# Kernel optimization log

Measured on AMD Instinct MI355X. Metric: run time of the kernel, lower is better.

## Reference

```python
import jax, jax.numpy as jnp
from jax import lax
import numpy as np

V = 4096                 # variants per batch
NUM_READ_FEATURES = 24
NUM_INFO_FEATURES = 10
REF_LEN = 25             # ref sequence length (one-hot over ACGT)
CONV_C = 32
KERN = 3
READ_E = 128
INFO_E = 64
SEQ_E = 64
EMB = READ_E + INFO_E + SEQ_E   # 256, matches hstack of read/info/seq embeddings
FFN = 512                # self_attention_hidden_dimension
NUM_BLOCKS = 2           # num_self_attention_layers
AGG_H = 256
AGG_OUT = 128
WEIGHT_RANGE = 0.2


def _init_params(key):
    ks = iter(jax.random.split(key, 40))
    def lin(din, dout):
        w = jax.random.normal(next(ks), (din, dout), jnp.float32) / np.float32(np.sqrt(din))
        return w, jnp.zeros((dout,), jnp.float32)
    p = {}
    p['read_w1'], p['read_b1'] = lin(NUM_READ_FEATURES, READ_E)
    p['read_w2'], p['read_b2'] = lin(READ_E, READ_E)
    p['info_w1'], p['info_b1'] = lin(NUM_INFO_FEATURES, INFO_E)
    p['info_w2'], p['info_b2'] = lin(INFO_E, INFO_E)
    p['conv_w'] = jax.random.normal(next(ks), (CONV_C, 4, KERN), jnp.float32) / np.float32(np.sqrt(4 * KERN))
    p['conv_b'] = jnp.zeros((CONV_C,), jnp.float32)
    flat = CONV_C * (REF_LEN - KERN + 1)
    p['seq_w'], p['seq_b'] = lin(flat, SEQ_E)
    p['blk_w1'] = jax.random.normal(next(ks), (NUM_BLOCKS, EMB, FFN), jnp.float32) / np.float32(np.sqrt(EMB))
    p['blk_b1'] = jnp.zeros((NUM_BLOCKS, FFN), jnp.float32)
    p['blk_wg'] = jax.random.normal(next(ks), (NUM_BLOCKS, EMB, FFN), jnp.float32) / np.float32(np.sqrt(EMB))
    p['blk_bg'] = jnp.zeros((NUM_BLOCKS, FFN), jnp.float32)
    p['blk_w2'] = jax.random.normal(next(ks), (NUM_BLOCKS, FFN, EMB), jnp.float32) / np.float32(np.sqrt(FFN))
    p['blk_b2'] = jnp.zeros((NUM_BLOCKS, EMB), jnp.float32)
    p['agg_w1'], p['agg_b1'] = lin(EMB, AGG_H)
    p['agg_w2'], p['agg_b2'] = lin(AGG_H, AGG_OUT)
    return p


def setup_inputs() -> dict:
    rng = np.random.default_rng(0)
    ref_counts_np = rng.integers(5, 45, size=V)
    alt_counts_np = rng.integers(2, 23, size=V)
    total_ref = int(ref_counts_np.sum())
    total_alt = int(alt_counts_np.sum())
    key = jax.random.key(0)
    k1, k2, k3, kp = jax.random.split(key, 4)
    reads_2d = jax.random.normal(k1, (total_ref + total_alt, NUM_READ_FEATURES), jnp.float32)
    info_2d = jax.random.normal(k2, (V, NUM_INFO_FEATURES), jnp.float32)
    base_idx = rng.integers(0, 4, size=(V, REF_LEN))
    ref_seq_oh = jnp.asarray(np.eye(4, dtype=np.float32)[base_idx].transpose(0, 2, 1))  # [V,4,L]
    alt_u = jax.random.uniform(k3, (total_alt,), jnp.float32)  # replaces torch.rand for alt weights
    inp = {
        'reads_2d': reads_2d, 'info_2d': info_2d, 'ref_seq_oh': ref_seq_oh, 'alt_u': alt_u,
        'ref_counts': jnp.asarray(ref_counts_np, jnp.int32),
        'alt_counts': jnp.asarray(alt_counts_np, jnp.int32),
    }
    inp.update(_init_params(kp))
    return inp


def _mlp2(x, w1, b1, w2, b2):
    return jax.nn.relu(x @ w1 + b1) @ w2 + b2


def _forward(reads_2d, info_2d, ref_seq_oh, alt_u,
             read_w1, read_b1, read_w2, read_b2,
             info_w1, info_b1, info_w2, info_b2,
             conv_w, conv_b, seq_w, seq_b,
             blk_w1, blk_b1, blk_wg, blk_bg, blk_w2, blk_b2,
             agg_w1, agg_b1, agg_w2, agg_b2,
             ref_counts, alt_counts):
    total_alt = alt_u.shape[0]
    total_ref = reads_2d.shape[0] - total_alt
    # per-read and per-variant embeddings
    read_re = _mlp2(reads_2d, read_w1, read_b1, read_w2, read_b2)          # [R, READ_E]
    info_ve = _mlp2(info_2d, info_w1, info_b1, info_w2, info_b2)           # [V, INFO_E]
    conv = lax.conv_general_dilated(ref_seq_oh, conv_w, window_strides=(1,), padding='VALID',
                                    dimension_numbers=('NCH', 'OIH', 'NCH'))
    conv = jax.nn.relu(conv + conv_b[None, :, None])                       # [V, C, L-K+1]
    seq_ve = conv.reshape(conv.shape[0], -1) @ seq_w + seq_b               # [V, SEQ_E]
    info_seq_ve = jnp.concatenate([info_ve, seq_ve], axis=1)               # [V, INFO_E+SEQ_E]
    # ragged broadcast: variant-level rows repeated per read (repeat_interleave)
    ref_ids = jnp.repeat(jnp.arange(V), ref_counts, total_repeat_length=total_ref)
    alt_ids = jnp.repeat(jnp.arange(V), alt_counts, total_repeat_length=total_alt)
    ref_x = jnp.concatenate([read_re[:total_ref], info_seq_ve[ref_ids]], axis=1)   # [total_ref, EMB]
    alt_x = jnp.concatenate([read_re[total_ref:], info_seq_ve[alt_ids]], axis=1)   # [total_alt, EMB]
    ref_cf = ref_counts.astype(ref_x.dtype)[:, None]
    alt_cf = alt_counts.astype(alt_x.dtype)[:, None]
    # gated ref/alt encoder: per-read MLP cross-gated by the other set's segment mean
    for i in range(NUM_BLOCKS):
        ref_mean = jax.ops.segment_sum(ref_x, ref_ids, num_segments=V) / ref_cf
        alt_mean = jax.ops.segment_sum(alt_x, alt_ids, num_segments=V) / alt_cf
        def blk(x, gate_src):
            h = jax.nn.relu(x @ blk_w1[i] + blk_b1[i]) * jax.nn.sigmoid(gate_src @ blk_wg[i] + blk_bg[i])
            return h @ blk_w2[i] + blk_b2[i]
        ref_x = ref_x + blk(ref_x, alt_mean[ref_ids])
        alt_x = alt_x + blk(alt_x, ref_mean[alt_ids])
    # normalized weighted segment sums over alt reads (utils.sums_over_rows)
    w_r = 1.0 + WEIGHT_RANGE * (1.0 - 2.0 * alt_u)                          # [total_alt]
    wt_sums_v = jax.ops.segment_sum(w_r, alt_ids, num_segments=V)           # [V]
    norm_w = w_r / wt_sums_v[alt_ids]
    alt_means_ve = jax.ops.segment_sum(alt_x * norm_w[:, None], alt_ids, num_segments=V)  # [V, EMB]
    return _mlp2(alt_means_ve, agg_w1, agg_b1, agg_w2, agg_b2)              # [V, AGG_OUT]


def reference(reads_2d, info_2d, ref_seq_oh, alt_u,
              read_w1, read_b1, read_w2, read_b2,
              info_w1, info_b1, info_w2, info_b2,
              conv_w, conv_b, seq_w, seq_b,
              blk_w1, blk_b1, blk_wg, blk_bg, blk_w2, blk_b2,
              agg_w1, agg_b1, agg_w2, agg_b2,
              ref_counts, alt_counts):
    return _forward(reads_2d, info_2d, ref_seq_oh, alt_u,
                    read_w1, read_b1, read_w2, read_b2,
                    info_w1, info_b1, info_w2, info_b2,
                    conv_w, conv_b, seq_w, seq_b,
                    blk_w1, blk_b1, blk_wg, blk_bg, blk_w2, blk_b2,
                    agg_w1, agg_b1, agg_w2, agg_b2,
                    ref_counts, alt_counts)
```

## Files before the change

kernel.cpp:

```cpp
#include <hip/hip_runtime.h>
#include <math.h>


typedef short short8 __attribute__((ext_vector_type(8)));
typedef __bf16 bf16x8 __attribute__((ext_vector_type(8)));
typedef float f32x4 __attribute__((ext_vector_type(4)));

__device__ inline unsigned short f2bf(float f) {
    unsigned u = __builtin_bit_cast(unsigned, f);
    u += 0x7fffu + ((u >> 16) & 1u);
    return (unsigned short)(u >> 16);
}
__device__ inline float bf2f(unsigned short u) {
    unsigned v = ((unsigned)u) << 16;
    return __builtin_bit_cast(float, v);
}

__device__ inline f32x4 mfma16(short8 a, short8 b, f32x4 c) {
    return __builtin_amdgcn_mfma_f32_16x16x32_bf16(
        __builtin_bit_cast(bf16x8, a), __builtin_bit_cast(bf16x8, b), c, 0, 0, 0);
}

__device__ inline int lds_idx(int row, int k, int Kp, int mask) {
    return row * Kp + (k ^ ((row & mask) << 3));
}

__global__ __launch_bounds__(256) void scan_counts(const int* __restrict__ cnt,
                                                   int* __restrict__ off, int V) {
    __shared__ int part[256];
    int t = threadIdx.x;
    int items = (V + 255) >> 8;
    int base = t * items;
    int s = 0;
    for (int i = 0; i < items; i++) {
        int idx = base + i;
        if (idx < V) s += cnt[idx];
    }
    part[t] = s;
    __syncthreads();
    for (int d = 1; d < 256; d <<= 1) {
        int v = (t >= d) ? part[t - d] : 0;
        __syncthreads();
        part[t] += v;
        __syncthreads();
    }
    int run = (t == 0) ? 0 : part[t - 1];
    for (int i = 0; i < items; i++) {
        int idx = base + i;
        if (idx < V) {
            off[idx] = run;
            run += cnt[idx];
        }
    }
    if (t == 255) off[V] = part[255];
}

__global__ void fill_ids(const int* __restrict__ off_r, int* __restrict__ rid_r,
                         const int* __restrict__ off_a, int* __restrict__ rid_a, int V) {
    int v = blockIdx.x * blockDim.x + threadIdx.x;
    if (v < V) {
        int s = off_r[v], e = off_r[v + 1];
        for (int r = s; r < e; r++) rid_r[r] = v;
    } else if (v < 2 * V) {
        int u = v - V;
        int s = off_a[u], e = off_a[u + 1];
        for (int r = s; r < e; r++) rid_a[r] = u;
    }
}

__global__ void pack_w(const float* __restrict__ src, unsigned short* __restrict__ dst,
                       int Ksrc, int K, int N, int ctN) {
    int idx = blockIdx.x * 256 + threadIdx.x;
    if (idx >= N * K) return;
    int e = idx & 7;
    int lane = (idx >> 3) & 63;
    int li = lane & 15, lg = lane >> 4;
    int r = idx >> 9;
    int ct = r % ctN;
    int r2 = r / ctN;
    int sN = K >> 5;
    int s = r2 % sN;
    int strip = r2 / sN;
    int n = strip * (ctN << 4) + (ct << 4) + li;
    int k = (s << 5) + (lg << 3) + e;
    dst[idx] = (k < Ksrc) ? f2bf(src[(size_t)k * N + n]) : (unsigned short)0;
}

__global__ void reads_to_bf(const float* __restrict__ reads, unsigned short* __restrict__ out,
                            int R) {
    int idx = blockIdx.x * 256 + threadIdx.x;
    if (idx >= R * 32) return;
    int r = idx >> 5, k = idx & 31;
    out[idx] = (k < 24) ? f2bf(reads[(size_t)r * 24 + k]) : (unsigned short)0;
}

template <int EPI>
__global__ __launch_bounds__(256, 4) void gemm_bf16(
        const unsigned short* __restrict__ A, const unsigned short* __restrict__ Bp,
        const float* __restrict__ bias, void* __restrict__ C0, void* __restrict__ C1,
        int M, int K, int mask, int ldc, int TR) {
    extern __shared__ unsigned short As[];
    const int m0 = blockIdx.x * 64, n0 = blockIdx.y * 64;
    const int tid = threadIdx.x;
    const int kc = K >> 3;
    for (int i = tid; i < (kc << 6); i += 256) {
        int r = i / kc, k8 = (i - r * kc) << 3;
        short8 v = {0, 0, 0, 0, 0, 0, 0, 0};
        if (m0 + r < M) v = *(const short8*)(A + (size_t)(m0 + r) * K + k8);
        *(short8*)&As[lds_idx(r, k8, K, mask)] = v;
    }
    __syncthreads();
    const int wid = tid >> 6, lane = tid & 63;
    const int lr = lane & 15, lg = lane >> 4;
    f32x4 acc[4];
#pragma unroll
    for (int ct = 0; ct < 4; ++ct) acc[ct] = f32x4{0.f, 0.f, 0.f, 0.f};
    const unsigned short* Bb = Bp + (size_t)blockIdx.y * ((size_t)K << 6) + (lane << 3);
    const int nk = K >> 5;
    for (int s = 0; s < nk; ++s) {
        int k0 = (s << 5) + (lg << 3);
        short8 af = *(const short8*)&As[lds_idx((wid << 4) + lr, k0, K, mask)];
#pragma unroll
        for (int ct = 0; ct < 4; ++ct) {
            short8 bf = *(const short8*)(Bb + (s << 11) + (ct << 9));
            acc[ct] = mfma16(af, bf, acc[ct]);
        }
    }
#pragma unroll
    for (int ct = 0; ct < 4; ++ct) {
        int c = n0 + (ct << 4) + lr;
        float bb = bias[c];
#pragma unroll
        for (int q = 0; q < 4; ++q) {
            int rg = m0 + (wid << 4) + (lg << 2) + q;
            if (rg >= M) continue;
            float v = acc[ct][q] + bb;
            if (EPI == 0) {
                ((float*)C0)[(size_t)rg * ldc + c] = v;
            } else if (EPI == 1) {
                ((unsigned short*)C0)[(size_t)rg * ldc + c] = f2bf(fmaxf(v, 0.f));
            } else if (EPI == 2) {
                ((unsigned short*)C0)[(size_t)rg * ldc + c] = f2bf(1.f / (1.f + __expf(-v)));
            } else {
                unsigned short* base = (rg < TR) ? ((unsigned short*)C0 + (size_t)rg * ldc)
                                                 : ((unsigned short*)C1 + (size_t)(rg - TR) * ldc);
                base[c] = f2bf(v);
            }
        }
    }
}

__global__ __launch_bounds__(128) void variant_embed(
        const float* __restrict__ info2d, const float* __restrict__ oh,
        const float* __restrict__ iw1, const float* __restrict__ ib1,
        const float* __restrict__ iw2, const float* __restrict__ ib2,
        const float* __restrict__ cw, const float* __restrict__ cb,
        const float* __restrict__ sw, const float* __restrict__ sb,
        unsigned short* __restrict__ isv, int V) {
    __shared__ float iw1s[10 * 64], iw2s[64 * 64], ib1s[64], ib2s[64];
    __shared__ float cws[32 * 4 * 3], cbs[32];
    __shared__ float ohs[100], cv[736], his[64], infs[10];
    int v = blockIdx.x;
    int t = threadIdx.x;
    for (int i = t; i < 640; i += 128) iw1s[i] = iw1[i];
    for (int i = t; i < 4096; i += 128) iw2s[i] = iw2[i];
    for (int i = t; i < 384; i += 128) cws[i] = cw[i];
    if (t < 64) { ib1s[t] = ib1[t]; ib2s[t] = ib2[t]; }
    if (t < 32) cbs[t] = cb[t];
    for (int i = t; i < 100; i += 128) ohs[i] = oh[(size_t)v * 100 + i];
    if (t < 10) infs[t] = info2d[(size_t)v * 10 + t];
    __syncthreads();
    for (int j = t; j < 736; j += 128) {
        int c = j / 23, p = j - c * 23;
        float a = cbs[c];
#pragma unroll
        for (int i = 0; i < 4; i++)
#pragma unroll
            for (int k = 0; k < 3; k++)
                a += cws[(c * 4 + i) * 3 + k] * ohs[i * 25 + p + k];
        cv[j] = fmaxf(a, 0.f);
    }
    if (t < 64) {
        float h = ib1s[t];
#pragma unroll
        for (int k = 0; k < 10; k++) h += infs[k] * iw1s[k * 64 + t];
        his[t] = fmaxf(h, 0.f);
    }
    __syncthreads();
    if (t < 64) {
        float o = ib2s[t];
        for (int k = 0; k < 64; k++) o += his[k] * iw2s[k * 64 + t];
        isv[(size_t)v * 128 + t] = f2bf(o);
    } else {
        int tt = t - 64;
        float s = sb[tt];
        for (int j = 0; j < 736; j++) s += cv[j] * sw[j * 64 + tt];
        isv[(size_t)v * 128 + 64 + tt] = f2bf(s);
    }
}

__global__ void gather_isv_bf(const uint4* __restrict__ isv4,
                              const int* __restrict__ rid_r, const int* __restrict__ rid_a,
                              uint4* __restrict__ xref4, uint4* __restrict__ xalt4,
                              int TR, int TA) {
    long idx = (long)blockIdx.x * blockDim.x + threadIdx.x;
    long total = (long)(TR + TA) * 16;
    if (idx >= total) return;
    int r = (int)(idx >> 4);
    int j = (int)(idx & 15);
    if (r < TR)
        xref4[(size_t)r * 32 + 16 + j] = isv4[(size_t)rid_r[r] * 16 + j];
    else {
        int r2 = r - TR;
        xalt4[(size_t)r2 * 32 + 16 + j] = isv4[(size_t)rid_a[r2] * 16 + j];
    }
}

__global__ __launch_bounds__(256) void seg_mean_bf(
        const unsigned short* __restrict__ xref, const int* __restrict__ off_r,
        const unsigned short* __restrict__ xalt, const int* __restrict__ off_a,
        unsigned short* __restrict__ m2, int V) {
    __shared__ float red[2048];
    int b = blockIdx.x;
    int t = threadIdx.x;
    const unsigned short* x;
    const int* off;
    unsigned short* out;
    int v;
    if (b < V) { x = xref; off = off_r; out = m2 + (size_t)(V + b) * 256; v = b; }
    else { x = xalt; off = off_a; out = m2 + (size_t)(b - V) * 256; v = b - V; }
    int s = off[v], e = off[v + 1];
    int g = t >> 5, c8 = (t & 31) << 3;
    float a[8] = {0.f, 0.f, 0.f, 0.f, 0.f, 0.f, 0.f, 0.f};
    for (int r = s + g; r < e; r += 8) {
        short8 vv = *(const short8*)(x + (size_t)r * 256 + c8);
#pragma unroll
        for (int k = 0; k < 8; k++) a[k] += bf2f((unsigned short)vv[k]);
    }
#pragma unroll
    for (int k = 0; k < 8; k++) red[g * 256 + c8 + k] = a[k];
    __syncthreads();
    float acc = red[t];
#pragma unroll
    for (int g2 = 1; g2 < 8; g2++) acc += red[g2 * 256 + t];
    out[t] = f2bf(acc / (float)(e - s));
}

__global__ __launch_bounds__(512, 4) void fused_block(
        unsigned short* __restrict__ xref, unsigned short* __restrict__ xalt,
        const unsigned short* __restrict__ W1p,
        const unsigned short* __restrict__ W2p,
        const float* __restrict__ b1, const float* __restrict__ b2,
        const unsigned short* __restrict__ gate_r, const unsigned short* __restrict__ gate_a,
        const int* __restrict__ rid_r, const int* __restrict__ rid_a,
        int TR, int TA, int ntr) {
    __shared__ unsigned short U[64 * 512];
    __shared__ int rid_s[64];
    float* OutF = (float*)U;
    const int nwg = gridDim.x;
    const int bid0 = blockIdx.x;
    const int q8 = nwg >> 3, r8 = nwg & 7;
    const int xcd = bid0 & 7;
    const int bid = (xcd < r8 ? xcd * (q8 + 1) : r8 * (q8 + 1) + (xcd - r8) * q8)
                    + (bid0 >> 3);
    const bool isref = bid < ntr;
    const int m0 = (isref ? bid : bid - ntr) * 64;
    const int M = isref ? TR : TA;
    unsigned short* x = isref ? xref : xalt;
    const unsigned short* gate = isref ? gate_r : gate_a;
    const int* rid = isref ? rid_r : rid_a;
    const int tid = threadIdx.x;
    if (tid < 64) rid_s[tid] = (m0 + tid < M) ? rid[m0 + tid] : 0;
#pragma unroll
    for (int u = 0; u < 4; ++u) {
        int i = tid + (u << 9);
        int r = i >> 5, j = i & 31;
        short8 v = {0, 0, 0, 0, 0, 0, 0, 0};
        if (m0 + r < M)
            v = *(const short8*)(x + (size_t)(m0 + r) * 256 + ((j ^ (r & 15)) << 3));
        *(short8*)&U[r * 256 + (j << 3)] = v;
    }
    __syncthreads();
    const int wid = tid >> 6, lane = tid & 63;
    const int li = lane & 15, lg = lane >> 4;
    const int ns = wid << 6;
    f32x4 acc1[4][4];
#pragma unroll
    for (int i = 0; i < 4; ++i)
#pragma unroll
        for (int j = 0; j < 4; ++j) acc1[i][j] = f32x4{0.f, 0.f, 0.f, 0.f};
    const unsigned short* W1b = W1p + ((size_t)wid << 14) + (lane << 3);
    short8 awc[4], awn[4];
#pragma unroll
    for (int ct = 0; ct < 4; ++ct) awc[ct] = *(const short8*)(W1b + (ct << 9));
#pragma unroll
    for (int s = 0; s < 8; ++s) {
        if (s < 7) {
#pragma unroll
            for (int ct = 0; ct < 4; ++ct)
                awn[ct] = *(const short8*)(W1b + ((s + 1) << 11) + (ct << 9));
        }
        int k0 = (s << 5) + (lg << 3);
        __builtin_amdgcn_s_setprio(1);
#pragma unroll
        for (int rt = 0; rt < 4; ++rt) {
            short8 bx = *(const short8*)&U[lds_idx(rt * 16 + li, k0, 256, 15)];
#pragma unroll
            for (int ct = 0; ct < 4; ++ct)
                acc1[rt][ct] = mfma16(awc[ct], bx, acc1[rt][ct]);
        }
        __builtin_amdgcn_s_setprio(0);
#pragma unroll
        for (int ct = 0; ct < 4; ++ct) awc[ct] = awn[ct];
    }
    __syncthreads();
#pragma unroll
    for (int rt = 0; rt < 4; ++rt) {
        int m = rt * 16 + li;
        const unsigned short* grow = gate + (size_t)rid_s[m] * 512 + ns + (lg << 2);
        const float* b1p = b1 + ns + (lg << 2);
#pragma unroll
        for (int ct = 0; ct < 4; ++ct) {
            uint2 gw = *(const uint2*)(grow + (ct << 4));
            float4 bv = *(const float4*)(b1p + (ct << 4));
            float g0 = bf2f((unsigned short)(gw.x & 0xffff));
            float g1 = bf2f((unsigned short)(gw.x >> 16));
            float g2 = bf2f((unsigned short)(gw.y & 0xffff));
            float g3 = bf2f((unsigned short)(gw.y >> 16));
            unsigned h0 = f2bf(fmaxf(acc1[rt][ct][0] + bv.x, 0.f) * g0);
            unsigned h1 = f2bf(fmaxf(acc1[rt][ct][1] + bv.y, 0.f) * g1);
            unsigned h2 = f2bf(fmaxf(acc1[rt][ct][2] + bv.z, 0.f) * g2);
            unsigned h3 = f2bf(fmaxf(acc1[rt][ct][3] + bv.w, 0.f) * g3);
            uint2 pk;
            pk.x = h0 | (h1 << 16);
            pk.y = h2 | (h3 << 16);
            int n = ns + (ct << 4) + (lg << 2);
            *(uint2*)&U[lds_idx(m, n, 512, 15)] = pk;
        }
    }
    __syncthreads();
    f32x4 acc2[4][2];
#pragma unroll
    for (int i = 0; i < 4; ++i)
#pragma unroll
        for (int j = 0; j < 2; ++j) acc2[i][j] = f32x4{0.f, 0.f, 0.f, 0.f};
    const unsigned short* W2b = W2p + ((size_t)wid << 14) + (lane << 3);
    short8 bwc[2], bwn[2];
#pragma unroll
    for (int ct = 0; ct < 2; ++ct) bwc[ct] = *(const short8*)(W2b + (ct << 9));
#pragma unroll
    for (int s = 0; s < 16; ++s) {
        if (s < 15) {
#pragma unroll
            for (int ct = 0; ct < 2; ++ct)
                bwn[ct] = *(const short8*)(W2b + ((s + 1) << 10) + (ct << 9));
        }
        int k0 = (s << 5) + (lg << 3);
        __builtin_amdgcn_s_setprio(1);
#pragma unroll
        for (int rt = 0; rt < 4; ++rt) {
            short8 ah = *(const short8*)&U[lds_idx(rt * 16 + li, k0, 512, 15)];
#pragma unroll
            for (int ct = 0; ct < 2; ++ct)
                acc2[rt][ct] = mfma16(ah, bwc[ct], acc2[rt][ct]);
        }
        __builtin_amdgcn_s_setprio(0);
#pragma unroll
        for (int ct = 0; ct < 2; ++ct) bwc[ct] = bwn[ct];
    }
    __syncthreads();
    const int cs = wid << 5;
#pragma unroll
    for (int ct = 0; ct < 2; ++ct) {
        int c = cs + (ct << 4) + li;
        float bb = b2[c];
#pragma unroll
        for (int rt = 0; rt < 4; ++rt)
#pragma unroll
            for (int q = 0; q < 4; ++q) {
                int m = rt * 16 + (lg << 2) + q;
                OutF[m * 256 + (c ^ (((m >> 2) & 3) << 3))] = acc2[rt][ct][q] + bb;
            }
    }
    __syncthreads();
#pragma unroll
    for (int u = 0; u < 4; ++u) {
        int i = tid + (u << 9);
        int r = i >> 5, j = i & 31;
        if (m0 + r >= M) continue;
        unsigned short* xp = x + (size_t)(m0 + r) * 256 + (j << 3);
        short8 xv = *(const short8*)xp;
        int c0 = (j << 3) ^ ((((r >> 2) & 3)) << 3);
        float4 f0 = *(const float4*)&OutF[r * 256 + c0];
        float4 f1 = *(const float4*)&OutF[r * 256 + c0 + 4];
        short8 o;
        o[0] = (short)f2bf(bf2f((unsigned short)xv[0]) + f0.x);
        o[1] = (short)f2bf(bf2f((unsigned short)xv[1]) + f0.y);
        o[2] = (short)f2bf(bf2f((unsigned short)xv[2]) + f0.z);
        o[3] = (short)f2bf(bf2f((unsigned short)xv[3]) + f0.w);
        o[4] = (short)f2bf(bf2f((unsigned short)xv[4]) + f1.x);
        o[5] = (short)f2bf(bf2f((unsigned short)xv[5]) + f1.y);
        o[6] = (short)f2bf(bf2f((unsigned short)xv[6]) + f1.z);
        o[7] = (short)f2bf(bf2f((unsigned short)xv[7]) + f1.w);
        *(short8*)xp = o;
    }
}

__global__ void alt_wsum(const float* __restrict__ au, const int* __restrict__ off_a,
                         float* __restrict__ wsum, int V) {
    int v = blockIdx.x * blockDim.x + threadIdx.x;
    if (v >= V) return;
    float s = 0.f;
    for (int r = off_a[v]; r < off_a[v + 1]; r++) s += 1.2f - 0.4f * au[r];
    wsum[v] = s;
}

__global__ __launch_bounds__(256) void alt_weighted_mean_bf(
        const unsigned short* __restrict__ xalt, const float* __restrict__ au,
        const int* __restrict__ off_a, const float* __restrict__ wsum,
        unsigned short* __restrict__ av, int V) {
    __shared__ float red[2048];
    int v = blockIdx.x;
    int t = threadIdx.x;
    int s = off_a[v], e = off_a[v + 1];
    float inv = 1.f / wsum[v];
    int g = t >> 5, c8 = (t & 31) << 3;
    float a[8] = {0.f, 0.f, 0.f, 0.f, 0.f, 0.f, 0.f, 0.f};
    for (int r = s + g; r < e; r += 8) {
        float w = (1.2f - 0.4f * au[r]) * inv;
        short8 vv = *(const short8*)(xalt + (size_t)r * 256 + c8);
#pragma unroll
        for (int k = 0; k < 8; k++) a[k] += bf2f((unsigned short)vv[k]) * w;
    }
#pragma unroll
    for (int k = 0; k < 8; k++) red[g * 256 + c8 + k] = a[k];
    __syncthreads();
    float acc = red[t];
#pragma unroll
    for (int g2 = 1; g2 < 8; g2++) acc += red[g2 * 256 + t];
    av[(size_t)v * 256 + t] = f2bf(acc);
}

extern "C" void kernel_launch(void* const* d_in, const int* in_sizes, int n_in,
                              void* d_out, int out_size, void* d_ws, size_t ws_size,
                              hipStream_t stream) {
    const float* reads = (const float*)d_in[0];
    const float* info2d = (const float*)d_in[1];
    const float* oh = (const float*)d_in[2];
    const float* au = (const float*)d_in[3];
    const int* ref_counts = (const int*)d_in[4];
    const int* alt_counts = (const int*)d_in[5];
    const float* rw1 = (const float*)d_in[6];
    const float* rb1 = (const float*)d_in[7];
    const float* rw2 = (const float*)d_in[8];
    const float* rb2 = (const float*)d_in[9];
    const float* iw1 = (const float*)d_in[10];
    const float* ib1 = (const float*)d_in[11];
    const float* iw2 = (const float*)d_in[12];
    const float* ib2 = (const float*)d_in[13];
    const float* cw = (const float*)d_in[14];
    const float* cb = (const float*)d_in[15];
    const float* sw = (const float*)d_in[16];
    const float* sb = (const float*)d_in[17];
    const float* blk_w1 = (const float*)d_in[18];
    const float* blk_b1 = (const float*)d_in[19];
    const float* blk_wg = (const float*)d_in[20];
    const float* blk_bg = (const float*)d_in[21];
    const float* blk_w2 = (const float*)d_in[22];
    const float* blk_b2 = (const float*)d_in[23];
    const float* agg_w1 = (const float*)d_in[24];
    const float* agg_b1 = (const float*)d_in[25];
    const float* agg_w2 = (const float*)d_in[26];
    const float* agg_b2 = (const float*)d_in[27];

    const int R = in_sizes[0] / 24;
    const int TA = in_sizes[3];
    const int TR = R - TA;
    const int V = in_sizes[4];

    size_t p = 0;
    auto carve = [&](size_t bytes) -> void* {
        void* q = (char*)d_ws + p;
        p = (p + bytes + 255) & ~(size_t)255;
        return q;
    };
    int* off_r = (int*)carve((V + 1) * sizeof(int));
    int* off_a = (int*)carve((V + 1) * sizeof(int));
    int* rid_r = (int*)carve((size_t)TR * sizeof(int));
    int* rid_a = (int*)carve((size_t)TA * sizeof(int));
    unsigned short* isv = (unsigned short*)carve((size_t)V * 128 * 2);
    unsigned short* xref = (unsigned short*)carve((size_t)TR * 256 * 2);
    unsigned short* xalt = (unsigned short*)carve((size_t)TA * 256 * 2);
    unsigned short* W1p0 = (unsigned short*)carve((size_t)512 * 256 * 2);
    unsigned short* W1p1 = (unsigned short*)carve((size_t)512 * 256 * 2);
    unsigned short* Wgp0 = (unsigned short*)carve((size_t)512 * 256 * 2);
    unsigned short* Wgp1 = (unsigned short*)carve((size_t)512 * 256 * 2);
    unsigned short* W2p0 = (unsigned short*)carve((size_t)256 * 512 * 2);
    unsigned short* W2p1 = (unsigned short*)carve((size_t)256 * 512 * 2);
    unsigned short* RW1p = (unsigned short*)carve((size_t)128 * 32 * 2);
    unsigned short* RW2p = (unsigned short*)carve((size_t)128 * 128 * 2);
    unsigned short* AG1p = (unsigned short*)carve((size_t)256 * 256 * 2);
    unsigned short* AG2p = (unsigned short*)carve((size_t)128 * 256 * 2);
    float* wsum = (float*)carve((size_t)V * sizeof(float));
    size_t mark = p;
    unsigned short* reads_bf = (unsigned short*)carve((size_t)R * 32 * 2);
    unsigned short* h1 = (unsigned short*)carve((size_t)R * 128 * 2);
    size_t endA = p;
    p = mark;
    unsigned short* m2 = (unsigned short*)carve((size_t)2 * V * 256 * 2);
    unsigned short* gate2 = (unsigned short*)carve((size_t)2 * V * 512 * 2);
    unsigned short* avb_bf = (unsigned short*)carve((size_t)V * 256 * 2);
    unsigned short* aggh_bf = (unsigned short*)carve((size_t)V * 256 * 2);
    if (endA > p) p = endA;
    (void)ws_size; (void)n_in; (void)out_size;

    scan_counts<<<1, 256, 0, stream>>>(ref_counts, off_r, V);
    scan_counts<<<1, 256, 0, stream>>>(alt_counts, off_a, V);
    fill_ids<<<(2 * V + 255) / 256, 256, 0, stream>>>(off_r, rid_r, off_a, rid_a, V);

    auto P = [&](const float* src, unsigned short* dst, int Ksrc, int K, int N, int ctN) {
        int tot = N * K;
        pack_w<<<(tot + 255) / 256, 256, 0, stream>>>(src, dst, Ksrc, K, N, ctN);
    };
    P(blk_w1, W1p0, 256, 256, 512, 4);
    P(blk_w1 + 256 * 512, W1p1, 256, 256, 512, 4);
    P(blk_wg, Wgp0, 256, 256, 512, 4);
    P(blk_wg + 256 * 512, Wgp1, 256, 256, 512, 4);
    P(blk_w2, W2p0, 512, 512, 256, 2);
    P(blk_w2 + 512 * 256, W2p1, 512, 512, 256, 2);
    P(rw1, RW1p, 24, 32, 128, 4);
    P(rw2, RW2p, 128, 128, 128, 4);
    P(agg_w1, AG1p, 256, 256, 256, 4);
    P(agg_w2, AG2p, 256, 256, 128, 4);

    reads_to_bf<<<(R * 32 + 255) / 256, 256, 0, stream>>>(reads, reads_bf, R);
    {
        dim3 g1((R + 63) / 64, 2);
        gemm_bf16<1><<<g1, 256, 64 * 32 * 2, stream>>>(reads_bf, RW1p, rb1, h1, nullptr,
                                                       R, 32, 3, 128, 0);
        gemm_bf16<3><<<g1, 256, 64 * 128 * 2, stream>>>(h1, RW2p, rb2, xref, xalt,
                                                        R, 128, 15, 256, TR);
    }

    variant_embed<<<V, 128, 0, stream>>>(info2d, oh, iw1, ib1, iw2, ib2, cw, cb, sw, sb, isv, V);
    long gtot = (long)R * 16;
    gather_isv_bf<<<(int)((gtot + 255) / 256), 256, 0, stream>>>(
        (const uint4*)isv, rid_r, rid_a, (uint4*)xref, (uint4*)xalt, TR, TA);

    const int ntr = (TR + 63) / 64, nta = (TA + 63) / 64;
    for (int it = 0; it < 2; ++it) {
        const unsigned short* W1p = it ? W1p1 : W1p0;
        const unsigned short* Wgp = it ? Wgp1 : Wgp0;
        const unsigned short* W2p = it ? W2p1 : W2p0;
        const float* B1 = blk_b1 + (size_t)it * 512;
        const float* Bg = blk_bg + (size_t)it * 512;
        const float* B2 = blk_b2 + (size_t)it * 256;

        seg_mean_bf<<<2 * V, 256, 0, stream>>>(xref, off_r, xalt, off_a, m2, V);
        dim3 gg(2 * V / 64, 8);
        gemm_bf16<2><<<gg, 256, 64 * 256 * 2, stream>>>(m2, Wgp, Bg, gate2, nullptr,
                                                        2 * V, 256, 15, 512, 0);
        fused_block<<<ntr + nta, 512, 0, stream>>>(xref, xalt, W1p, W2p, B1, B2,
                                                   gate2, gate2 + (size_t)V * 512,
                                                   rid_r, rid_a, TR, TA, ntr);
    }

    alt_wsum<<<(V + 255) / 256, 256, 0, stream>>>(au, off_a, wsum, V);
    alt_weighted_mean_bf<<<V, 256, 0, stream>>>(xalt, au, off_a, wsum, avb_bf, V);
    {
        dim3 ga(V / 64, 4);
        gemm_bf16<1><<<ga, 256, 64 * 256 * 2, stream>>>(avb_bf, AG1p, agg_b1, aggh_bf, nullptr,
                                                        V, 256, 15, 256, 0);
        dim3 go(V / 64, 2);
        gemm_bf16<0><<<go, 256, 64 * 256 * 2, stream>>>(aggh_bf, AG2p, agg_b2, d_out, nullptr,
                                                        V, 256, 15, 128, 0);
    }
}
```

Measured before the change: 494.0 us.

## Fuse read MLP with ISV gather, merge packing and scan kernels

Replaces the reads-to-bf16 conversion, two read-MLP GEMMs and the ISV gather with one fused kernel that keeps the hidden layer in LDS and writes the full embedding rows directly. It also merges the two scans with fill_ids, merges the ten weight-pack launches into one, and folds alt_wsum into the weighted-mean kernel. Separately, it drops the W1 register double-buffering in fused_block. The aim is fewer launches and no round trips of intermediates through global memory; the fused kernel trades this for more LDS per block, and the fill inside the scan kernel now runs on only two blocks.

After: 455.6 us. 1.08x faster.

```diff
diff --git a/kernel.cpp b/kernel.cpp
--- a/kernel.cpp
+++ b/kernel.cpp
@@ -25,9 +25,14 @@
     return row * Kp + (k ^ ((row & mask) << 3));
 }
 
-__global__ __launch_bounds__(256) void scan_counts(const int* __restrict__ cnt,
-                                                   int* __restrict__ off, int V) {
+__global__ __launch_bounds__(256) void scan_fill(
+        const int* __restrict__ cref, const int* __restrict__ calt,
+        int* __restrict__ off_r, int* __restrict__ off_a,
+        int* __restrict__ rid_r, int* __restrict__ rid_a, int V) {
     __shared__ int part[256];
+    const int* cnt = blockIdx.x ? calt : cref;
+    int* off = blockIdx.x ? off_a : off_r;
+    int* rid = blockIdx.x ? rid_a : rid_r;
     int t = threadIdx.x;
     int items = (V + 255) >> 8;
     int base = t * items;
@@ -53,29 +58,20 @@
         }
     }
     if (t == 255) off[V] = part[255];
-}
-
-__global__ void fill_ids(const int* __restrict__ off_r, int* __restrict__ rid_r,
-                         const int* __restrict__ off_a, int* __restrict__ rid_a, int V) {
-    int v = blockIdx.x * blockDim.x + threadIdx.x;
-    if (v < V) {
-        int s = off_r[v], e = off_r[v + 1];
-        for (int r = s; r < e; r++) rid_r[r] = v;
-    } else if (v < 2 * V) {
-        int u = v - V;
-        int s = off_a[u], e = off_a[u + 1];
-        for (int r = s; r < e; r++) rid_a[r] = u;
-    }
-}
-
-__global__ void pack_w(const float* __restrict__ src, unsigned short* __restrict__ dst,
-                       int Ksrc, int K, int N, int ctN) {
-    int idx = blockIdx.x * 256 + threadIdx.x;
-    if (idx >= N * K) return;
-    int e = idx & 7;
-    int lane = (idx >> 3) & 63;
+    __syncthreads();
+    for (int v = t; v < V; v += 256) {
+        int s0 = off[v], e0 = off[v + 1];
+        for (int r = s0; r < e0; r++) rid[r] = v;
+    }
+}
+
+__device__ inline void pack_one(const float* __restrict__ src,
+                                unsigned short* __restrict__ dst, int i,
+                                int Ksrc, int K, int N, int ctN) {
+    int e = i & 7;
+    int lane = (i >> 3) & 63;
     int li = lane & 15, lg = lane >> 4;
-    int r = idx >> 9;
+    int r = i >> 9;
     int ct = r % ctN;
     int r2 = r / ctN;
     int sN = K >> 5;
@@ -83,22 +79,37 @@
     int strip = r2 / sN;
     int n = strip * (ctN << 4) + (ct << 4) + li;
     int k = (s << 5) + (lg << 3) + e;
-    dst[idx] = (k < Ksrc) ? f2bf(src[(size_t)k * N + n]) : (unsigned short)0;
-}
-
-__global__ void reads_to_bf(const float* __restrict__ reads, unsigned short* __restrict__ out,
-                            int R) {
+    dst[i] = (k < Ksrc) ? f2bf(src[(size_t)k * N + n]) : (unsigned short)0;
+}
+
+__global__ __launch_bounds__(256) void pack_all(
+        const float* __restrict__ w1, const float* __restrict__ wg,
+        const float* __restrict__ w2, const float* __restrict__ rw1,
+        const float* __restrict__ rw2, const float* __restrict__ ag1,
+        const float* __restrict__ ag2,
+        unsigned short* W1p0, unsigned short* W1p1,
+        unsigned short* Wgp0, unsigned short* Wgp1,
+        unsigned short* W2p0, unsigned short* W2p1,
+        unsigned short* RW1p, unsigned short* RW2p,
+        unsigned short* AG1p, unsigned short* AG2p) {
     int idx = blockIdx.x * 256 + threadIdx.x;
-    if (idx >= R * 32) return;
-    int r = idx >> 5, k = idx & 31;
-    out[idx] = (k < 24) ? f2bf(reads[(size_t)r * 24 + k]) : (unsigned short)0;
+    if (idx < 131072)       pack_one(w1,          W1p0, idx,          256, 256, 512, 4);
+    else if (idx < 262144)  pack_one(w1 + 131072, W1p1, idx - 131072, 256, 256, 512, 4);
+    else if (idx < 393216)  pack_one(wg,          Wgp0, idx - 262144, 256, 256, 512, 4);
+    else if (idx < 524288)  pack_one(wg + 131072, Wgp1, idx - 393216, 256, 256, 512, 4);
+    else if (idx < 655360)  pack_one(w2,          W2p0, idx - 524288, 512, 512, 256, 2);
+    else if (idx < 786432)  pack_one(w2 + 131072, W2p1, idx - 655360, 512, 512, 256, 2);
+    else if (idx < 790528)  pack_one(rw1,         RW1p, idx - 786432, 24, 32, 128, 1);
+    else if (idx < 806912)  pack_one(rw2,         RW2p, idx - 790528, 128, 128, 128, 1);
+    else if (idx < 872448)  pack_one(ag1,         AG1p, idx - 806912, 256, 256, 256, 4);
+    else if (idx < 905216)  pack_one(ag2,         AG2p, idx - 872448, 256, 256, 128, 4);
 }
 
 template <int EPI>
 __global__ __launch_bounds__(256, 4) void gemm_bf16(
         const unsigned short* __restrict__ A, const unsigned short* __restrict__ Bp,
-        const float* __restrict__ bias, void* __restrict__ C0, void* __restrict__ C1,
-        int M, int K, int mask, int ldc, int TR) {
+        const float* __restrict__ bias, void* __restrict__ C0,
+        int M, int K, int mask, int ldc) {
     extern __shared__ unsigned short As[];
     const int m0 = blockIdx.x * 64, n0 = blockIdx.y * 64;
     const int tid = threadIdx.x;
@@ -139,14 +150,103 @@
                 ((float*)C0)[(size_t)rg * ldc + c] = v;
             } else if (EPI == 1) {
                 ((unsigned short*)C0)[(size_t)rg * ldc + c] = f2bf(fmaxf(v, 0.f));
-            } else if (EPI == 2) {
+            } else {
                 ((unsigned short*)C0)[(size_t)rg * ldc + c] = f2bf(1.f / (1.f + __expf(-v)));
-            } else {
-                unsigned short* base = (rg < TR) ? ((unsigned short*)C0 + (size_t)rg * ldc)
-                                                 : ((unsigned short*)C1 + (size_t)(rg - TR) * ldc);
-                base[c] = f2bf(v);
             }
         }
+    }
+}
+
+__global__ __launch_bounds__(512) void read_mlp_fused(
+        const float* __restrict__ reads,
+        const unsigned short* __restrict__ RW1p, const unsigned short* __restrict__ RW2p,
+        const float* __restrict__ rb1, const float* __restrict__ rb2,
+        const uint4* __restrict__ isv4,
+        const int* __restrict__ rid_r, const int* __restrict__ rid_a,
+        unsigned short* __restrict__ xref, unsigned short* __restrict__ xalt,
+        int R, int TR) {
+    __shared__ unsigned short Xs[64 * 32];
+    __shared__ unsigned short Hs[64 * 128];
+    __shared__ int rid_s[64];
+    const int m0 = blockIdx.x * 64;
+    const int tid = threadIdx.x;
+    if (tid < 64) {
+        int g = m0 + tid;
+        rid_s[tid] = (g < R) ? (g < TR ? rid_r[g] : rid_a[g - TR]) : 0;
+    }
+    if (tid < 256) {
+        int r = tid >> 2, c8 = (tid & 3) << 3;
+        short8 v = {0, 0, 0, 0, 0, 0, 0, 0};
+        int g = m0 + r;
+        if (g < R && c8 < 24) {
+            const float* sp = reads + (size_t)g * 24 + c8;
+#pragma unroll
+            for (int e = 0; e < 8; e++) v[e] = (short)f2bf(sp[e]);
+        }
+        *(short8*)&Xs[lds_idx(r, c8, 32, 3)] = v;
+    }
+    __syncthreads();
+    const int wid = tid >> 6, lane = tid & 63;
+    const int li = lane & 15, lg = lane >> 4;
+    f32x4 a1[4];
+#pragma unroll
+    for (int rt = 0; rt < 4; ++rt) a1[rt] = f32x4{0.f, 0.f, 0.f, 0.f};
+    short8 bw1 = *(const short8*)(RW1p + ((size_t)wid << 9) + (lane << 3));
+#pragma unroll
+    for (int rt = 0; rt < 4; ++rt) {
+        short8 af = *(const short8*)&Xs[lds_idx(rt * 16 + li, lg << 3, 32, 3)];
+        a1[rt] = mfma16(af, bw1, a1[rt]);
+    }
+    float b1v = rb1[(wid << 4) + li];
+#pragma unroll
+    for (int rt = 0; rt < 4; ++rt)
+#pragma unroll
+        for (int q = 0; q < 4; ++q) {
+            int row = rt * 16 + (lg << 2) + q;
+            Hs[lds_idx(row, (wid << 4) + li, 128, 15)] = f2bf(fmaxf(a1[rt][q] + b1v, 0.f));
+        }
+    __syncthreads();
+    f32x4 a2[4];
+#pragma unroll
+    for (int rt = 0; rt < 4; ++rt) a2[rt] = f32x4{0.f, 0.f, 0.f, 0.f};
+    const unsigned short* B2 = RW2p + ((size_t)wid << 11) + (lane << 3);
+#pragma unroll
+    for (int s = 0; s < 4; ++s) {
+        short8 bw = *(const short8*)(B2 + (s << 9));
+        int k0 = (s << 5) + (lg << 3);
+#pragma unroll
+        for (int rt = 0; rt < 4; ++rt) {
+            short8 ah = *(const short8*)&Hs[lds_idx(rt * 16 + li, k0, 128, 15)];
+            a2[rt] = mfma16(ah, bw, a2[rt]);
+        }
+    }
+    float b2v = rb2[(wid << 4) + li];
+    unsigned short ov[4][4];
+#pragma unroll
+    for (int rt = 0; rt < 4; ++rt)
+#pragma unroll
+        for (int q = 0; q < 4; ++q) ov[rt][q] = f2bf(a2[rt][q] + b2v);
+    __syncthreads();
+#pragma unroll
+    for (int rt = 0; rt < 4; ++rt)
+#pragma unroll
+        for (int q = 0; q < 4; ++q) {
+            int row = rt * 16 + (lg << 2) + q;
+            Hs[row * 128 + (wid << 4) + li] = ov[rt][q];
+        }
+    __syncthreads();
+#pragma unroll
+    for (int u = 0; u < 4; ++u) {
+        int i = tid + (u << 9);
+        int r = i >> 5, j = i & 31;
+        int g = m0 + r;
+        if (g >= R) continue;
+        unsigned short* dst = (g < TR) ? (xref + (size_t)g * 256)
+                                       : (xalt + (size_t)(g - TR) * 256);
+        if (j < 16)
+            *(short8*)(dst + (j << 3)) = *(const short8*)&Hs[r * 128 + (j << 3)];
+        else
+            ((uint4*)(dst + 128))[j - 16] = isv4[(size_t)rid_s[r] * 16 + (j - 16)];
     }
 }
 
@@ -196,23 +296,6 @@
         float s = sb[tt];
         for (int j = 0; j < 736; j++) s += cv[j] * sw[j * 64 + tt];
         isv[(size_t)v * 128 + 64 + tt] = f2bf(s);
-    }
-}
-
-__global__ void gather_isv_bf(const uint4* __restrict__ isv4,
-                              const int* __restrict__ rid_r, const int* __restrict__ rid_a,
-                              uint4* __restrict__ xref4, uint4* __restrict__ xalt4,
-                              int TR, int TA) {
-    long idx = (long)blockIdx.x * blockDim.x + threadIdx.x;
-    long total = (long)(TR + TA) * 16;
-    if (idx >= total) return;
-    int r = (int)(idx >> 4);
-    int j = (int)(idx & 15);
-    if (r < TR)
-        xref4[(size_t)r * 32 + 16 + j] = isv4[(size_t)rid_r[r] * 16 + j];
-    else {
-        int r2 = r - TR;
-        xalt4[(size_t)r2 * 32 + 16 + j] = isv4[(size_t)rid_a[r2] * 16 + j];
     }
 }
 
@@ -290,16 +373,12 @@
 #pragma unroll
         for (int j = 0; j < 4; ++j) acc1[i][j] = f32x4{0.f, 0.f, 0.f, 0.f};
     const unsigned short* W1b = W1p + ((size_t)wid << 14) + (lane << 3);
-    short8 awc[4], awn[4];
-#pragma unroll
-    for (int ct = 0; ct < 4; ++ct) awc[ct] = *(const short8*)(W1b + (ct << 9));
 #pragma unroll
     for (int s = 0; s < 8; ++s) {
-        if (s < 7) {
-#pragma unroll
-            for (int ct = 0; ct < 4; ++ct)
-                awn[ct] = *(const short8*)(W1b + ((s + 1) << 11) + (ct << 9));
-        }
+        short8 awc[4];
+#pragma unroll
+        for (int ct = 0; ct < 4; ++ct)
+            awc[ct] = *(const short8*)(W1b + (s << 11) + (ct << 9));
         int k0 = (s << 5) + (lg << 3);
         __builtin_amdgcn_s_setprio(1);
 #pragma unroll
@@ -310,8 +389,6 @@
                 acc1[rt][ct] = mfma16(awc[ct], bx, acc1[rt][ct]);
         }
         __builtin_amdgcn_s_setprio(0);
-#pragma unroll
-        for (int ct = 0; ct < 4; ++ct) awc[ct] = awn[ct];
     }
     __syncthreads();
 #pragma unroll
@@ -406,24 +483,23 @@
     }
 }
 
-__global__ void alt_wsum(const float* __restrict__ au, const int* __restrict__ off_a,
-                         float* __restrict__ wsum, int V) {
-    int v = blockIdx.x * blockDim.x + threadIdx.x;
-    if (v >= V) return;
-    float s = 0.f;
-    for (int r = off_a[v]; r < off_a[v + 1]; r++) s += 1.2f - 0.4f * au[r];
-    wsum[v] = s;
-}
-
 __global__ __launch_bounds__(256) void alt_weighted_mean_bf(
         const unsigned short* __restrict__ xalt, const float* __restrict__ au,
-        const int* __restrict__ off_a, const float* __restrict__ wsum,
-        unsigned short* __restrict__ av, int V) {
+        const int* __restrict__ off_a, unsigned short* __restrict__ av, int V) {
     __shared__ float red[2048];
+    __shared__ float wred[256];
     int v = blockIdx.x;
     int t = threadIdx.x;
     int s = off_a[v], e = off_a[v + 1];
-    float inv = 1.f / wsum[v];
+    float wp = 0.f;
+    for (int r = s + t; r < e; r += 256) wp += 1.2f - 0.4f * au[r];
+    wred[t] = wp;
+    __syncthreads();
+    for (int d = 128; d; d >>= 1) {
+        if (t < d) wred[t] += wred[t + d];
+        __syncthreads();
+    }
+    float inv = 1.f / wred[0];
     int g = t >> 5, c8 = (t & 31) << 3;
     float a[8] = {0.f, 0.f, 0.f, 0.f, 0.f, 0.f, 0.f, 0.f};
     for (int r = s + g; r < e; r += 8) {
@@ -501,51 +577,20 @@
     unsigned short* RW2p = (unsigned short*)carve((size_t)128 * 128 * 2);
     unsigned short* AG1p = (unsigned short*)carve((size_t)256 * 256 * 2);
     unsigned short* AG2p = (unsigned short*)carve((size_t)128 * 256 * 2);
-    float* wsum = (float*)carve((size_t)V * sizeof(float));
-    size_t mark = p;
-    unsigned short* reads_bf = (unsigned short*)carve((size_t)R * 32 * 2);
-    unsigned short* h1 = (unsigned short*)carve((size_t)R * 128 * 2);
-    size_t endA = p;
-    p = mark;
     unsigned short* m2 = (unsigned short*)carve((size_t)2 * V * 256 * 2);
     unsigned short* gate2 = (unsigned short*)carve((size_t)2 * V * 512 * 2);
     unsigned short* avb_bf = (unsigned short*)carve((size_t)V * 256 * 2);
     unsigned short* aggh_bf = (unsigned short*)carve((size_t)V * 256 * 2);
-    if (endA > p) p = endA;
     (void)ws_size; (void)n_in; (void)out_size;
 
-    scan_counts<<<1, 256, 0, stream>>>(ref_counts, off_r, V);
-    scan_counts<<<1, 256, 0, stream>>>(alt_counts, off_a, V);
-    fill_ids<<<(2 * V + 255) / 256, 256, 0, stream>>>(off_r, rid_r, off_a, rid_a, V);
-
-    auto P = [&](const float* src, unsigned short* dst, int Ksrc, int K, int N, int ctN) {
-        int tot = N * K;
-        pack_w<<<(tot + 255) / 256, 256, 0, stream>>>(src, dst, Ksrc, K, N, ctN);
-    };
-    P(blk_w1, W1p0, 256, 256, 512, 4);
-    P(blk_w1 + 256 * 512, W1p1, 256, 256, 512, 4);
-    P(blk_wg, Wgp0, 256, 256, 512, 4);
-    P(blk_wg + 256 * 512, Wgp1, 256, 256, 512, 4);
-    P(blk_w2, W2p0, 512, 512, 256, 2);
-    P(blk_w2 + 512 * 256, W2p1, 512, 512, 256, 2);
-    P(rw1, RW1p, 24, 32, 128, 4);
-    P(rw2, RW2p, 128, 128, 128, 4);
-    P(agg_w1, AG1p, 256, 256, 256, 4);
-    P(agg_w2, AG2p, 256, 256, 128, 4);
-
-    reads_to_bf<<<(R * 32 + 255) / 256, 256, 0, stream>>>(reads, reads_bf, R);
-    {
-        dim3 g1((R + 63) / 64, 2);
-        gemm_bf16<1><<<g1, 256, 64 * 32 * 2, stream>>>(reads_bf, RW1p, rb1, h1, nullptr,
-                                                       R, 32, 3, 128, 0);
-        gemm_bf16<3><<<g1, 256, 64 * 128 * 2, stream>>>(h1, RW2p, rb2, xref, xalt,
-                                                        R, 128, 15, 256, TR);
-    }
-
+    scan_fill<<<2, 256, 0, stream>>>(ref_counts, alt_counts, off_r, off_a, rid_r, rid_a, V);
+    pack_all<<<3536, 256, 0, stream>>>(blk_w1, blk_wg, blk_w2, rw1, rw2, agg_w1, agg_w2,
+                                       W1p0, W1p1, Wgp0, Wgp1, W2p0, W2p1,
+                                       RW1p, RW2p, AG1p, AG2p);
     variant_embed<<<V, 128, 0, stream>>>(info2d, oh, iw1, ib1, iw2, ib2, cw, cb, sw, sb, isv, V);
-    long gtot = (long)R * 16;
-    gather_isv_bf<<<(int)((gtot + 255) / 256), 256, 0, stream>>>(
-        (const uint4*)isv, rid_r, rid_a, (uint4*)xref, (uint4*)xalt, TR, TA);
+
+    read_mlp_fused<<<(R + 63) / 64, 512, 0, stream>>>(
+        reads, RW1p, RW2p, rb1, rb2, (const uint4*)isv, rid_r, rid_a, xref, xalt, R, TR);
 
     const int ntr = (TR + 63) / 64, nta = (TA + 63) / 64;
     for (int it = 0; it < 2; ++it) {
@@ -558,21 +603,20 @@
 
         seg_mean_bf<<<2 * V, 256, 0, stream>>>(xref, off_r, xalt, off_a, m2, V);
         dim3 gg(2 * V / 64, 8);
-        gemm_bf16<2><<<gg, 256, 64 * 256 * 2, stream>>>(m2, Wgp, Bg, gate2, nullptr,
-                                                        2 * V, 256, 15, 512, 0);
+        gemm_bf16<2><<<gg, 256, 64 * 256 * 2, stream>>>(m2, Wgp, Bg, gate2,
+                                                        2 * V, 256, 15, 512);
         fused_block<<<ntr + nta, 512, 0, stream>>>(xref, xalt, W1p, W2p, B1, B2,
                                                    gate2, gate2 + (size_t)V * 512,
                                                    rid_r, rid_a, TR, TA, ntr);
     }
 
-    alt_wsum<<<(V + 255) / 256, 256, 0, stream>>>(au, off_a, wsum, V);
-    alt_weighted_mean_bf<<<V, 256, 0, stream>>>(xalt, au, off_a, wsum, avb_bf, V);
+    alt_weighted_mean_bf<<<V, 256, 0, stream>>>(xalt, au, off_a, avb_bf, V);
     {
         dim3 ga(V / 64, 4);
-        gemm_bf16<1><<<ga, 256, 64 * 256 * 2, stream>>>(avb_bf, AG1p, agg_b1, aggh_bf, nullptr,
-                                                        V, 256, 15, 256, 0);
+        gemm_bf16<1><<<ga, 256, 64 * 256 * 2, stream>>>(avb_bf, AG1p, agg_b1, aggh_bf,
+                                                        V, 256, 15, 256);
         dim3 go(V / 64, 2);
-        gemm_bf16<0><<<go, 256, 64 * 256 * 2, stream>>>(aggh_bf, AG2p, agg_b2, d_out, nullptr,
-                                                        V, 256, 15, 128, 0);
-    }
-}
+        gemm_bf16<0><<<go, 256, 64 * 256 * 2, stream>>>(aggh_bf, AG2p, agg_b2, d_out,
+                                                        V, 256, 15, 128);
+    }
+}
```
